# Performance work log

Hardware: AMD Instinct MI355X
Metric: run time of the kernel (lower is better)

## Reference

```python
import jax, jax.numpy as jnp
import numpy as np

CODEBOOK_SIZE = 8192
DIM = 64
B, N = 4, 4096


def setup_inputs() -> dict:
    key = jax.random.key(0)
    k1, k2 = jax.random.split(key)
    x = jax.random.normal(k1, (B, N, DIM), dtype=jnp.float32)
    node_mask = jnp.ones((B, N), dtype=jnp.float32)
    embed = jax.random.normal(k2, (CODEBOOK_SIZE, DIM), dtype=jnp.float32)
    return {"x": x, "node_mask": node_mask, "embed": embed}


def reference(x, node_mask, embed):
    # x: [B, N, D]; embed: [K, D]; node_mask: [B, N]
    b, n, d = x.shape
    k = embed.shape[0]
    flatten = x.reshape(-1, d)  # [B*N, D]
    dist = -(
        jnp.sum(flatten * flatten, axis=1, keepdims=True)
        - 2.0 * (flatten @ embed.T)
        + jnp.sum(embed * embed, axis=1)[None, :]
    )
    embed_ind = jnp.argmax(dist, axis=-1)  # [B*N] nearest-code assignment
    quantize = embed[embed_ind].reshape(b, n, d)  # codebook gather
    # masked one-hot stats (embed_onehot * node_mask), via segment_sum
    mask_flat = node_mask.reshape(-1)
    counts = jax.ops.segment_sum(mask_flat, embed_ind, num_segments=k)  # [K]
    avg_probs = counts / jnp.asarray(flatten.shape[0], dtype=x.dtype)
    perplexity = jnp.exp(-jnp.sum(avg_probs * jnp.log(avg_probs + 1e-10)))
    return quantize, embed_ind.reshape(b, n), perplexity
```

## Files before the change

kernel.cpp:

```cpp
#include <hip/hip_runtime.h>

typedef __attribute__((ext_vector_type(8))) short short8;
typedef __attribute__((ext_vector_type(4))) float f32x4;

#define ROWS 16384
#define DIM 64
#define NCODES 8192
#define MARGIN 0.008f
#define KT_FB 256
#define CTS_PER_BLOCK 32
#define CHUNK 4

#define WS_BEST   0
#define WS_COUNTS 131072
#define WS_ENH    163840
#define WS_ESWZ   196608
#define WS_NEED   2293760

__device__ __forceinline__ unsigned long long pack_score(float s, int idx) {
  unsigned u = __float_as_uint(s);
  u ^= (unsigned)((int)u >> 31) | 0x80000000u;
  return ((unsigned long long)u << 32) | (unsigned)(0xFFFF - idx);
}
__device__ __forceinline__ unsigned short bf16hi(float f) {
  unsigned u = __float_as_uint(f);
  return (unsigned short)((u + 0x7FFFu + ((u >> 16) & 1u)) >> 16);
}

__global__ void vq_enorm(const float* __restrict__ embed, float* __restrict__ enh) {
  int k = blockIdx.x * 256 + threadIdx.x;
  const float4* e4 = (const float4*)(embed + (size_t)k * DIM);
  float a = 0.f, b = 0.f, c = 0.f, d = 0.f;
#pragma unroll
  for (int i = 0; i < DIM / 4; ++i) {
    float4 v = e4[i];
    a = fmaf(v.x, v.x, a); b = fmaf(v.y, v.y, b);
    c = fmaf(v.z, v.z, c); d = fmaf(v.w, v.w, d);
  }
  enh[k] = 0.5f * ((a + b) + (c + d));
}

__global__ void vq_prep_e(const float* __restrict__ embed, short* __restrict__ eswz) {
  int u = blockIdx.x * 256 + threadIdx.x;
  int l = u & 63, kc = (u >> 6) & 1, ct = u >> 7;
  int code = ct * 16 + (l & 15);
  int kb = kc * 32 + (l >> 4) * 8;
  const float* er = embed + (size_t)code * DIM + kb;
  short8 h8, l8;
#pragma unroll
  for (int j = 0; j < 8; ++j) {
    float v = er[j];
    unsigned short h = bf16hi(v);
    float r = v - __uint_as_float((unsigned)h << 16);
    h8[j] = (short)h;
    l8[j] = (short)bf16hi(r);
  }
  short8* dst = (short8*)eswz;
  size_t frag = (size_t)ct * 4 + kc * 2;
  dst[(frag + 0) * 64 + l] = h8;
  dst[(frag + 1) * 64 + l] = l8;
}

__global__ __launch_bounds__(256, 4) void vq_screen(
    const float* __restrict__ x, const float* __restrict__ embed,
    const short* __restrict__ eswz, const float* __restrict__ enh,
    unsigned long long* __restrict__ best) {
  const int t = threadIdx.x;
  const int l = t & 63, wid = t >> 6;
  const int cl = l & 15, grp = l >> 4;
  const int row0 = blockIdx.x * 128 + wid * 32;
  const int ct0 = blockIdx.y * CTS_PER_BLOCK;

  __shared__ short8 bstage[2][CHUNK * 4 * 64];
  __shared__ float enh_s[CTS_PER_BLOCK * 16];

  const char* gbase = (const char*)eswz + (size_t)ct0 * 4 * 1024;

  {
    char* lb = (char*)&bstage[0][0];
#pragma unroll
    for (int i = 0; i < 4; ++i) {
      const int e = i * 256 + t;
      __builtin_amdgcn_global_load_lds(
          (const __attribute__((address_space(1))) void*)(gbase + (size_t)e * 16),
          (__attribute__((address_space(3))) void*)(lb + e * 16), 16, 0, 0);
    }
  }

  enh_s[t] = enh[ct0 * 16 + t];
  enh_s[256 + t] = enh[ct0 * 16 + 256 + t];

  short8 ahi[2][2], alo[2][2];
#pragma unroll
  for (int s = 0; s < 2; ++s) {
    const float4* xr4 = (const float4*)(x + (size_t)(row0 + s * 16 + cl) * DIM);
#pragma unroll
    for (int kc = 0; kc < 2; ++kc) {
      const int q = kc * 8 + grp * 2;
      float4 v0 = xr4[q], v1 = xr4[q + 1];
      float vv[8] = {v0.x, v0.y, v0.z, v0.w, v1.x, v1.y, v1.z, v1.w};
#pragma unroll
      for (int j = 0; j < 8; ++j) {
        unsigned short h = bf16hi(vv[j]);
        float r = vv[j] - __uint_as_float((unsigned)h << 16);
        ahi[s][kc][j] = (short)h;
        alo[s][kc][j] = (short)bf16hi(r);
      }
    }
  }

  float bsc[2][4];
  int bidx[2][4];
#pragma unroll
  for (int s = 0; s < 2; ++s)
#pragma unroll
    for (int j = 0; j < 4; ++j) { bsc[s][j] = -3.4e38f; bidx[s][j] = 0; }

  __syncthreads();

#pragma unroll
  for (int ch = 0; ch < CTS_PER_BLOCK / CHUNK; ++ch) {
    const int cur = ch & 1;
    if (ch + 1 < CTS_PER_BLOCK / CHUNK) {
      const char* gb = gbase + (size_t)(ch + 1) * CHUNK * 4 * 1024;
      char* lb = (char*)&bstage[cur ^ 1][0];
#pragma unroll
      for (int i = 0; i < 4; ++i) {
        const int e = i * 256 + t;
        __builtin_amdgcn_global_load_lds(
            (const __attribute__((address_space(1))) void*)(gb + (size_t)e * 16),
            (__attribute__((address_space(3))) void*)(lb + e * 16), 16, 0, 0);
      }
    }

    const short8* bs = &bstage[cur][0];
#pragma unroll
    for (int ci = 0; ci < CHUNK; ++ci) {
      const int ctl = ch * CHUNK + ci;
      const float eh = enh_s[ctl * 16 + cl];
      short8 h0 = bs[(ci * 4 + 0) * 64 + l], l0 = bs[(ci * 4 + 1) * 64 + l];
      short8 h1 = bs[(ci * 4 + 2) * 64 + l], l1 = bs[(ci * 4 + 3) * 64 + l];

      f32x4 a00 = {-eh, -eh, -eh, -eh};
      f32x4 a10 = a00;
      f32x4 a01 = {0.f, 0.f, 0.f, 0.f};
      f32x4 a11 = a01;
      a00 = __builtin_amdgcn_mfma_f32_16x16x32_bf16(ahi[0][0], h0, a00, 0, 0, 0);
      a10 = __builtin_amdgcn_mfma_f32_16x16x32_bf16(ahi[1][0], h0, a10, 0, 0, 0);
      a01 = __builtin_amdgcn_mfma_f32_16x16x32_bf16(ahi[0][1], h1, a01, 0, 0, 0);
      a11 = __builtin_amdgcn_mfma_f32_16x16x32_bf16(ahi[1][1], h1, a11, 0, 0, 0);
      a00 = __builtin_amdgcn_mfma_f32_16x16x32_bf16(alo[0][0], h0, a00, 0, 0, 0);
      a10 = __builtin_amdgcn_mfma_f32_16x16x32_bf16(alo[1][0], h0, a10, 0, 0, 0);
      a01 = __builtin_amdgcn_mfma_f32_16x16x32_bf16(alo[0][1], h1, a01, 0, 0, 0);
      a11 = __builtin_amdgcn_mfma_f32_16x16x32_bf16(alo[1][1], h1, a11, 0, 0, 0);
      a00 = __builtin_amdgcn_mfma_f32_16x16x32_bf16(ahi[0][0], l0, a00, 0, 0, 0);
      a10 = __builtin_amdgcn_mfma_f32_16x16x32_bf16(ahi[1][0], l0, a10, 0, 0, 0);
      a01 = __builtin_amdgcn_mfma_f32_16x16x32_bf16(ahi[0][1], l1, a01, 0, 0, 0);
      a11 = __builtin_amdgcn_mfma_f32_16x16x32_bf16(ahi[1][1], l1, a11, 0, 0, 0);

      f32x4 s0 = a00 + a01;
      f32x4 s1 = a10 + a11;
      const int code = (ct0 + ctl) * 16 + cl;
#pragma unroll
      for (int j = 0; j < 4; ++j) {
        if (s0[j] > bsc[0][j]) { bsc[0][j] = s0[j]; bidx[0][j] = code; }
        if (s1[j] > bsc[1][j]) { bsc[1][j] = s1[j]; bidx[1][j] = code; }
      }
    }
    __syncthreads();
  }

  unsigned fmask = 0;
#pragma unroll
  for (int s = 0; s < 2; ++s)
#pragma unroll
    for (int j = 0; j < 4; ++j) {
      float m = bsc[s][j];
      m = fmaxf(m, __shfl_xor(m, 1));
      m = fmaxf(m, __shfl_xor(m, 2));
      m = fmaxf(m, __shfl_xor(m, 4));
      m = fmaxf(m, __shfl_xor(m, 8));
      if (bsc[s][j] >= m - MARGIN) fmask |= 1u << (s * 4 + j);
    }

  float exact[2][4];
#pragma unroll
  for (int s = 0; s < 2; ++s)
#pragma unroll
    for (int j = 0; j < 4; ++j) exact[s][j] = -3.4e38f;

  while (__any((int)(fmask != 0))) {
    const bool act = fmask != 0;
    const int sel = act ? __ffs(fmask) - 1 : 0;
    int code = 0;
#pragma unroll
    for (int s = 0; s < 2; ++s)
#pragma unroll
      for (int j = 0; j < 4; ++j)
        code = (sel == s * 4 + j) ? bidx[s][j] : code;
    int row = act ? (row0 + (sel >> 2) * 16 + grp * 4 + (sel & 3)) : row0;
    if (!act) code = 0;
    const float4* xr = (const float4*)(x + (size_t)row * DIM);
    const float4* er = (const float4*)(embed + (size_t)code * DIM);
    float a0 = 0, a1 = 0, a2 = 0, a3 = 0, n0 = 0, n1 = 0, n2 = 0, n3 = 0;
#pragma unroll
    for (int i = 0; i < 16; ++i) {
      float4 xv = xr[i], ev = er[i];
      a0 = fmaf(xv.x, ev.x, a0); a1 = fmaf(xv.y, ev.y, a1);
      a2 = fmaf(xv.z, ev.z, a2); a3 = fmaf(xv.w, ev.w, a3);
      n0 = fmaf(ev.x, ev.x, n0); n1 = fmaf(ev.y, ev.y, n1);
      n2 = fmaf(ev.z, ev.z, n2); n3 = fmaf(ev.w, ev.w, n3);
    }
    float ex = ((a0 + a1) + (a2 + a3)) - 0.5f * ((n0 + n1) + (n2 + n3));
#pragma unroll
    for (int s = 0; s < 2; ++s)
#pragma unroll
      for (int j = 0; j < 4; ++j)
        exact[s][j] = (act && sel == s * 4 + j) ? ex : exact[s][j];
    fmask = act ? (fmask & (fmask - 1)) : 0u;
  }

#pragma unroll
  for (int s = 0; s < 2; ++s)
#pragma unroll
    for (int j = 0; j < 4; ++j) {
      unsigned long long pk = pack_score(exact[s][j], bidx[s][j]);
      unsigned long long o;
      o = __shfl_xor(pk, 1); pk = pk > o ? pk : o;
      o = __shfl_xor(pk, 2); pk = pk > o ? pk : o;
      o = __shfl_xor(pk, 4); pk = pk > o ? pk : o;
      o = __shfl_xor(pk, 8); pk = pk > o ? pk : o;
      if (cl == 0) atomicMax(&best[row0 + s * 16 + grp * 4 + j], pk);
    }
}

__global__ __launch_bounds__(256, 2) void vq_score_fb(
    const float* __restrict__ x, const float* __restrict__ embed,
    const float* __restrict__ enh, unsigned long long* __restrict__ best) {
  const int row = blockIdx.x * 256 + threadIdx.x;
  const int c0 = blockIdx.y * KT_FB;
  float4 xa[16];
  const float4* xg = (const float4*)(x + (size_t)row * DIM);
#pragma unroll
  for (int i = 0; i < 16; ++i) xa[i] = xg[i];
  float bs = -3.4e38f;
  int bc = 0;
#pragma unroll 2
  for (int c = c0; c < c0 + KT_FB; ++c) {
    const float4* e4 = (const float4*)(embed + (size_t)c * DIM);
    float a0 = 0.f, a1 = 0.f, a2 = 0.f, a3 = 0.f;
#pragma unroll
    for (int i = 0; i < 16; ++i) {
      float4 ev = e4[i];
      a0 = fmaf(xa[i].x, ev.x, a0); a1 = fmaf(xa[i].y, ev.y, a1);
      a2 = fmaf(xa[i].z, ev.z, a2); a3 = fmaf(xa[i].w, ev.w, a3);
    }
    float s = ((a0 + a1) + (a2 + a3)) - enh[c];
    if (s > bs) { bs = s; bc = c; }
  }
  atomicMax(&best[row], pack_score(bs, bc));
}

__global__ void vq_finalize(const unsigned long long* __restrict__ best,
                            const float* __restrict__ embed,
                            const float* __restrict__ node_mask,
                            float* __restrict__ quant,
                            float* __restrict__ out_idx,
                            float* __restrict__ counts) {
  int gid = blockIdx.x * 256 + threadIdx.x;
  int row = gid >> 6, d = gid & 63;
  unsigned long long p = best[row];
  int idx = 0xFFFF - (int)(p & 0xFFFFull);
  quant[gid] = embed[(size_t)idx * DIM + d];
  if (d == 0) {
    out_idx[row] = (float)idx;
    atomicAdd(&counts[idx], node_mask[row]);
  }
}

__global__ void vq_perplexity(const float* __restrict__ counts, float* __restrict__ out) {
  int tid = threadIdx.x;
  float acc = 0.f;
  for (int k = tid; k < NCODES; k += 256) {
    float p = counts[k] * (1.0f / (float)ROWS);
    acc += p * logf(p + 1e-10f);
  }
#pragma unroll
  for (int off = 32; off > 0; off >>= 1) acc += __shfl_down(acc, off);
  __shared__ float red[4];
  if ((tid & 63) == 0) red[tid >> 6] = acc;
  __syncthreads();
  if (tid == 0) out[0] = expf(-((red[0] + red[1]) + (red[2] + red[3])));
}

extern "C" void kernel_launch(void* const* d_in, const int* in_sizes, int n_in,
                              void* d_out, int out_size, void* d_ws, size_t ws_size,
                              hipStream_t stream) {
  const float* x = (const float*)d_in[0];
  const float* node_mask = (const float*)d_in[1];
  const float* embed = (const float*)d_in[2];

  float* out = (float*)d_out;
  float* quant = out;
  float* out_idx = out + (size_t)ROWS * DIM;
  float* out_ppl = out_idx + ROWS;

  unsigned long long* best = (unsigned long long*)((char*)d_ws + WS_BEST);
  float* counts = (float*)((char*)d_ws + WS_COUNTS);
  float* enh = (float*)((char*)d_ws + WS_ENH);
  short* eswz = (short*)((char*)d_ws + WS_ESWZ);

  hipMemsetAsync(d_ws, 0, WS_ENH, stream);
  vq_enorm<<<NCODES / 256, 256, 0, stream>>>(embed, enh);
  if (ws_size >= WS_NEED) {
    vq_prep_e<<<256, 256, 0, stream>>>(embed, eswz);
    vq_screen<<<dim3(ROWS / 128, NCODES / (CTS_PER_BLOCK * 16)), 256, 0, stream>>>(
        x, embed, eswz, enh, best);
  } else {
    vq_score_fb<<<dim3(ROWS / 256, NCODES / KT_FB), 256, 0, stream>>>(x, embed, enh, best);
  }
  vq_finalize<<<ROWS * DIM / 256, 256, 0, stream>>>(best, embed, node_mask, quant, out_idx, counts);
  vq_perplexity<<<1, 256, 0, stream>>>(counts, out_ppl);
}
```

Measured before the change: 108.0 us.

## Replace LDS-staged codebook pipeline with direct register prefetch from global

The screening kernel no longer stages swizzled codebook fragments through double-buffered LDS with global_load_lds and block barriers. Each wave now loads its B fragments and norms straight from global memory into registers, prefetching the next code tile one iteration ahead. This removes the LDS traffic and __syncthreads. In exchange, all four waves in a block load the same fragments redundantly from global/L2, and register pressure rises.

```diff
diff --git a/kernel.cpp b/kernel.cpp
--- a/kernel.cpp
+++ b/kernel.cpp
@@ -9,7 +9,6 @@
 #define MARGIN 0.008f
 #define KT_FB 256
 #define CTS_PER_BLOCK 32
-#define CHUNK 4
 
 #define WS_BEST   0
 #define WS_COUNTS 131072
@@ -71,25 +70,6 @@
   const int row0 = blockIdx.x * 128 + wid * 32;
   const int ct0 = blockIdx.y * CTS_PER_BLOCK;
 
-  __shared__ short8 bstage[2][CHUNK * 4 * 64];
-  __shared__ float enh_s[CTS_PER_BLOCK * 16];
-
-  const char* gbase = (const char*)eswz + (size_t)ct0 * 4 * 1024;
-
-  {
-    char* lb = (char*)&bstage[0][0];
-#pragma unroll
-    for (int i = 0; i < 4; ++i) {
-      const int e = i * 256 + t;
-      __builtin_amdgcn_global_load_lds(
-          (const __attribute__((address_space(1))) void*)(gbase + (size_t)e * 16),
-          (__attribute__((address_space(3))) void*)(lb + e * 16), 16, 0, 0);
-    }
-  }
-
-  enh_s[t] = enh[ct0 * 16 + t];
-  enh_s[256 + t] = enh[ct0 * 16 + 256 + t];
-
   short8 ahi[2][2], alo[2][2];
 #pragma unroll
   for (int s = 0; s < 2; ++s) {
@@ -116,58 +96,50 @@
 #pragma unroll
     for (int j = 0; j < 4; ++j) { bsc[s][j] = -3.4e38f; bidx[s][j] = 0; }
 
-  __syncthreads();
-
-#pragma unroll
-  for (int ch = 0; ch < CTS_PER_BLOCK / CHUNK; ++ch) {
-    const int cur = ch & 1;
-    if (ch + 1 < CTS_PER_BLOCK / CHUNK) {
-      const char* gb = gbase + (size_t)(ch + 1) * CHUNK * 4 * 1024;
-      char* lb = (char*)&bstage[cur ^ 1][0];
-#pragma unroll
-      for (int i = 0; i < 4; ++i) {
-        const int e = i * 256 + t;
-        __builtin_amdgcn_global_load_lds(
-            (const __attribute__((address_space(1))) void*)(gb + (size_t)e * 16),
-            (__attribute__((address_space(3))) void*)(lb + e * 16), 16, 0, 0);
-      }
-    }
-
-    const short8* bs = &bstage[cur][0];
-#pragma unroll
-    for (int ci = 0; ci < CHUNK; ++ci) {
-      const int ctl = ch * CHUNK + ci;
-      const float eh = enh_s[ctl * 16 + cl];
-      short8 h0 = bs[(ci * 4 + 0) * 64 + l], l0 = bs[(ci * 4 + 1) * 64 + l];
-      short8 h1 = bs[(ci * 4 + 2) * 64 + l], l1 = bs[(ci * 4 + 3) * 64 + l];
-
-      f32x4 a00 = {-eh, -eh, -eh, -eh};
-      f32x4 a10 = a00;
-      f32x4 a01 = {0.f, 0.f, 0.f, 0.f};
-      f32x4 a11 = a01;
-      a00 = __builtin_amdgcn_mfma_f32_16x16x32_bf16(ahi[0][0], h0, a00, 0, 0, 0);
-      a10 = __builtin_amdgcn_mfma_f32_16x16x32_bf16(ahi[1][0], h0, a10, 0, 0, 0);
-      a01 = __builtin_amdgcn_mfma_f32_16x16x32_bf16(ahi[0][1], h1, a01, 0, 0, 0);
-      a11 = __builtin_amdgcn_mfma_f32_16x16x32_bf16(ahi[1][1], h1, a11, 0, 0, 0);
-      a00 = __builtin_amdgcn_mfma_f32_16x16x32_bf16(alo[0][0], h0, a00, 0, 0, 0);
-      a10 = __builtin_amdgcn_mfma_f32_16x16x32_bf16(alo[1][0], h0, a10, 0, 0, 0);
-      a01 = __builtin_amdgcn_mfma_f32_16x16x32_bf16(alo[0][1], h1, a01, 0, 0, 0);
-      a11 = __builtin_amdgcn_mfma_f32_16x16x32_bf16(alo[1][1], h1, a11, 0, 0, 0);
-      a00 = __builtin_amdgcn_mfma_f32_16x16x32_bf16(ahi[0][0], l0, a00, 0, 0, 0);
-      a10 = __builtin_amdgcn_mfma_f32_16x16x32_bf16(ahi[1][0], l0, a10, 0, 0, 0);
-      a01 = __builtin_amdgcn_mfma_f32_16x16x32_bf16(ahi[0][1], l1, a01, 0, 0, 0);
-      a11 = __builtin_amdgcn_mfma_f32_16x16x32_bf16(ahi[1][1], l1, a11, 0, 0, 0);
-
-      f32x4 s0 = a00 + a01;
-      f32x4 s1 = a10 + a11;
-      const int code = (ct0 + ctl) * 16 + cl;
-#pragma unroll
-      for (int j = 0; j < 4; ++j) {
-        if (s0[j] > bsc[0][j]) { bsc[0][j] = s0[j]; bidx[0][j] = code; }
-        if (s1[j] > bsc[1][j]) { bsc[1][j] = s1[j]; bidx[1][j] = code; }
-      }
-    }
-    __syncthreads();
+  const short8* eb = (const short8*)eswz + (size_t)ct0 * 4 * 64;
+
+  short8 h0 = eb[l], l0 = eb[64 + l], h1 = eb[128 + l], l1 = eb[192 + l];
+  float eh = enh[ct0 * 16 + cl];
+
+#pragma unroll
+  for (int ci = 0; ci < CTS_PER_BLOCK; ++ci) {
+    short8 nh0, nl0, nh1, nl1;
+    float neh;
+    if (ci + 1 < CTS_PER_BLOCK) {
+      const short8* nb = eb + (size_t)(ci + 1) * 256;
+      nh0 = nb[l]; nl0 = nb[64 + l]; nh1 = nb[128 + l]; nl1 = nb[192 + l];
+      neh = enh[(ct0 + ci + 1) * 16 + cl];
+    }
+
+    f32x4 a00 = {-eh, -eh, -eh, -eh};
+    f32x4 a10 = a00;
+    f32x4 a01 = {0.f, 0.f, 0.f, 0.f};
+    f32x4 a11 = a01;
+    a00 = __builtin_amdgcn_mfma_f32_16x16x32_bf16(ahi[0][0], h0, a00, 0, 0, 0);
+    a10 = __builtin_amdgcn_mfma_f32_16x16x32_bf16(ahi[1][0], h0, a10, 0, 0, 0);
+    a01 = __builtin_amdgcn_mfma_f32_16x16x32_bf16(ahi[0][1], h1, a01, 0, 0, 0);
+    a11 = __builtin_amdgcn_mfma_f32_16x16x32_bf16(ahi[1][1], h1, a11, 0, 0, 0);
+    a00 = __builtin_amdgcn_mfma_f32_16x16x32_bf16(alo[0][0], h0, a00, 0, 0, 0);
+    a10 = __builtin_amdgcn_mfma_f32_16x16x32_bf16(alo[1][0], h0, a10, 0, 0, 0);
+    a01 = __builtin_amdgcn_mfma_f32_16x16x32_bf16(alo[0][1], h1, a01, 0, 0, 0);
+    a11 = __builtin_amdgcn_mfma_f32_16x16x32_bf16(alo[1][1], h1, a11, 0, 0, 0);
+    a00 = __builtin_amdgcn_mfma_f32_16x16x32_bf16(ahi[0][0], l0, a00, 0, 0, 0);
+    a10 = __builtin_amdgcn_mfma_f32_16x16x32_bf16(ahi[1][0], l0, a10, 0, 0, 0);
+    a01 = __builtin_amdgcn_mfma_f32_16x16x32_bf16(ahi[0][1], l1, a01, 0, 0, 0);
+    a11 = __builtin_amdgcn_mfma_f32_16x16x32_bf16(ahi[1][1], l1, a11, 0, 0, 0);
+
+    f32x4 s0 = a00 + a01;
+    f32x4 s1 = a10 + a11;
+    const int code = (ct0 + ci) * 16 + cl;
+#pragma unroll
+    for (int j = 0; j < 4; ++j) {
+      if (s0[j] > bsc[0][j]) { bsc[0][j] = s0[j]; bidx[0][j] = code; }
+      if (s1[j] > bsc[1][j]) { bsc[1][j] = s1[j]; bidx[1][j] = code; }
+    }
+
+    if (ci + 1 < CTS_PER_BLOCK) {
+      h0 = nh0; l0 = nl0; h1 = nh1; l1 = nl1; eh = neh;
+    }
   }
 
   unsigned fmask = 0;
```

Measured after the change: 118.5 us. 1.1x slower.

## Halve rows per wave in screen kernel to raise occupancy

Applied to the files above, without the earlier changes.

Each wave in vq_screen now handles 16 rows instead of 32, so it keeps half the A fragments and best-score registers. The launch bound rises to 8 blocks per CU and the grid doubles. The LDS stage shrinks to 2 code tiles per chunk, the chunk loop is no longer unrolled, and code norms are read straight from global memory instead of a shared copy. In exchange, each B fragment loaded from LDS is reused by half as many MFMAs, and the codebook is streamed twice as many times overall.

```diff
diff --git a/kernel.cpp b/kernel.cpp
--- a/kernel.cpp
+++ b/kernel.cpp
@@ -9,7 +9,7 @@
 #define MARGIN 0.008f
 #define KT_FB 256
 #define CTS_PER_BLOCK 32
-#define CHUNK 4
+#define CCH 2
 
 #define WS_BEST   0
 #define WS_COUNTS 131072
@@ -61,25 +61,24 @@
   dst[(frag + 1) * 64 + l] = l8;
 }
 
-__global__ __launch_bounds__(256, 4) void vq_screen(
+__global__ __launch_bounds__(256, 8) void vq_screen(
     const float* __restrict__ x, const float* __restrict__ embed,
     const short* __restrict__ eswz, const float* __restrict__ enh,
     unsigned long long* __restrict__ best) {
   const int t = threadIdx.x;
   const int l = t & 63, wid = t >> 6;
   const int cl = l & 15, grp = l >> 4;
-  const int row0 = blockIdx.x * 128 + wid * 32;
+  const int row0 = blockIdx.x * 64 + wid * 16;
   const int ct0 = blockIdx.y * CTS_PER_BLOCK;
 
-  __shared__ short8 bstage[2][CHUNK * 4 * 64];
-  __shared__ float enh_s[CTS_PER_BLOCK * 16];
+  __shared__ short8 bstage[2][CCH * 4 * 64];
 
   const char* gbase = (const char*)eswz + (size_t)ct0 * 4 * 1024;
 
   {
     char* lb = (char*)&bstage[0][0];
 #pragma unroll
-    for (int i = 0; i < 4; ++i) {
+    for (int i = 0; i < CCH; ++i) {
       const int e = i * 256 + t;
       __builtin_amdgcn_global_load_lds(
           (const __attribute__((address_space(1))) void*)(gbase + (size_t)e * 16),
@@ -87,13 +86,9 @@
     }
   }
 
-  enh_s[t] = enh[ct0 * 16 + t];
-  enh_s[256 + t] = enh[ct0 * 16 + 256 + t];
-
-  short8 ahi[2][2], alo[2][2];
-#pragma unroll
-  for (int s = 0; s < 2; ++s) {
-    const float4* xr4 = (const float4*)(x + (size_t)(row0 + s * 16 + cl) * DIM);
+  short8 ahi[2], alo[2];
+  {
+    const float4* xr4 = (const float4*)(x + (size_t)(row0 + cl) * DIM);
 #pragma unroll
     for (int kc = 0; kc < 2; ++kc) {
       const int q = kc * 8 + grp * 2;
@@ -103,29 +98,26 @@
       for (int j = 0; j < 8; ++j) {
         unsigned short h = bf16hi(vv[j]);
         float r = vv[j] - __uint_as_float((unsigned)h << 16);
-        ahi[s][kc][j] = (short)h;
-        alo[s][kc][j] = (short)bf16hi(r);
+        ahi[kc][j] = (short)h;
+        alo[kc][j] = (short)bf16hi(r);
       }
     }
   }
 
-  float bsc[2][4];
-  int bidx[2][4];
-#pragma unroll
-  for (int s = 0; s < 2; ++s)
-#pragma unroll
-    for (int j = 0; j < 4; ++j) { bsc[s][j] = -3.4e38f; bidx[s][j] = 0; }
+  float bsc[4];
+  int bidx[4];
+#pragma unroll
+  for (int j = 0; j < 4; ++j) { bsc[j] = -3.4e38f; bidx[j] = 0; }
 
   __syncthreads();
 
-#pragma unroll
-  for (int ch = 0; ch < CTS_PER_BLOCK / CHUNK; ++ch) {
+  for (int ch = 0; ch < CTS_PER_BLOCK / CCH; ++ch) {
     const int cur = ch & 1;
-    if (ch + 1 < CTS_PER_BLOCK / CHUNK) {
-      const char* gb = gbase + (size_t)(ch + 1) * CHUNK * 4 * 1024;
+    if (ch + 1 < CTS_PER_BLOCK / CCH) {
+      const char* gb = gbase + (size_t)(ch + 1) * CCH * 4 * 1024;
       char* lb = (char*)&bstage[cur ^ 1][0];
 #pragma unroll
-      for (int i = 0; i < 4; ++i) {
+      for (int i = 0; i < CCH; ++i) {
         const int e = i * 256 + t;
         __builtin_amdgcn_global_load_lds(
             (const __attribute__((address_space(1))) void*)(gb + (size_t)e * 16),
@@ -135,36 +127,24 @@
 
     const short8* bs = &bstage[cur][0];
 #pragma unroll
-    for (int ci = 0; ci < CHUNK; ++ci) {
-      const int ctl = ch * CHUNK + ci;
-      const float eh = enh_s[ctl * 16 + cl];
-      short8 h0 = bs[(ci * 4 + 0) * 64 + l], l0 = bs[(ci * 4 + 1) * 64 + l];
-      short8 h1 = bs[(ci * 4 + 2) * 64 + l], l1 = bs[(ci * 4 + 3) * 64 + l];
-
-      f32x4 a00 = {-eh, -eh, -eh, -eh};
-      f32x4 a10 = a00;
-      f32x4 a01 = {0.f, 0.f, 0.f, 0.f};
-      f32x4 a11 = a01;
-      a00 = __builtin_amdgcn_mfma_f32_16x16x32_bf16(ahi[0][0], h0, a00, 0, 0, 0);
-      a10 = __builtin_amdgcn_mfma_f32_16x16x32_bf16(ahi[1][0], h0, a10, 0, 0, 0);
-      a01 = __builtin_amdgcn_mfma_f32_16x16x32_bf16(ahi[0][1], h1, a01, 0, 0, 0);
-      a11 = __builtin_amdgcn_mfma_f32_16x16x32_bf16(ahi[1][1], h1, a11, 0, 0, 0);
-      a00 = __builtin_amdgcn_mfma_f32_16x16x32_bf16(alo[0][0], h0, a00, 0, 0, 0);
-      a10 = __builtin_amdgcn_mfma_f32_16x16x32_bf16(alo[1][0], h0, a10, 0, 0, 0);
-      a01 = __builtin_amdgcn_mfma_f32_16x16x32_bf16(alo[0][1], h1, a01, 0, 0, 0);
-      a11 = __builtin_amdgcn_mfma_f32_16x16x32_bf16(alo[1][1], h1, a11, 0, 0, 0);
-      a00 = __builtin_amdgcn_mfma_f32_16x16x32_bf16(ahi[0][0], l0, a00, 0, 0, 0);
-      a10 = __builtin_amdgcn_mfma_f32_16x16x32_bf16(ahi[1][0], l0, a10, 0, 0, 0);
-      a01 = __builtin_amdgcn_mfma_f32_16x16x32_bf16(ahi[0][1], l1, a01, 0, 0, 0);
-      a11 = __builtin_amdgcn_mfma_f32_16x16x32_bf16(ahi[1][1], l1, a11, 0, 0, 0);
-
-      f32x4 s0 = a00 + a01;
-      f32x4 s1 = a10 + a11;
-      const int code = (ct0 + ctl) * 16 + cl;
+    for (int cil = 0; cil < CCH; ++cil) {
+      const int ci = ch * CCH + cil;
+      const float eh = enh[(ct0 + ci) * 16 + cl];
+      short8 h0 = bs[(cil * 4 + 0) * 64 + l], l0 = bs[(cil * 4 + 1) * 64 + l];
+      short8 h1 = bs[(cil * 4 + 2) * 64 + l], l1 = bs[(cil * 4 + 3) * 64 + l];
+
+      f32x4 acc = {-eh, -eh, -eh, -eh};
+      acc = __builtin_amdgcn_mfma_f32_16x16x32_bf16(ahi[0], h0, acc, 0, 0, 0);
+      acc = __builtin_amdgcn_mfma_f32_16x16x32_bf16(alo[0], h0, acc, 0, 0, 0);
+      acc = __builtin_amdgcn_mfma_f32_16x16x32_bf16(ahi[0], l0, acc, 0, 0, 0);
+      acc = __builtin_amdgcn_mfma_f32_16x16x32_bf16(ahi[1], h1, acc, 0, 0, 0);
+      acc = __builtin_amdgcn_mfma_f32_16x16x32_bf16(alo[1], h1, acc, 0, 0, 0);
+      acc = __builtin_amdgcn_mfma_f32_16x16x32_bf16(ahi[1], l1, acc, 0, 0, 0);
+
+      const int code = (ct0 + ci) * 16 + cl;
 #pragma unroll
       for (int j = 0; j < 4; ++j) {
-        if (s0[j] > bsc[0][j]) { bsc[0][j] = s0[j]; bidx[0][j] = code; }
-        if (s1[j] > bsc[1][j]) { bsc[1][j] = s1[j]; bidx[1][j] = code; }
+        if (acc[j] > bsc[j]) { bsc[j] = acc[j]; bidx[j] = code; }
       }
     }
     __syncthreads();
@@ -172,33 +152,26 @@
 
   unsigned fmask = 0;
 #pragma unroll
-  for (int s = 0; s < 2; ++s)
-#pragma unroll
-    for (int j = 0; j < 4; ++j) {
-      float m = bsc[s][j];
-      m = fmaxf(m, __shfl_xor(m, 1));
-      m = fmaxf(m, __shfl_xor(m, 2));
-      m = fmaxf(m, __shfl_xor(m, 4));
-      m = fmaxf(m, __shfl_xor(m, 8));
-      if (bsc[s][j] >= m - MARGIN) fmask |= 1u << (s * 4 + j);
-    }
-
-  float exact[2][4];
-#pragma unroll
-  for (int s = 0; s < 2; ++s)
-#pragma unroll
-    for (int j = 0; j < 4; ++j) exact[s][j] = -3.4e38f;
+  for (int j = 0; j < 4; ++j) {
+    float m = bsc[j];
+    m = fmaxf(m, __shfl_xor(m, 1));
+    m = fmaxf(m, __shfl_xor(m, 2));
+    m = fmaxf(m, __shfl_xor(m, 4));
+    m = fmaxf(m, __shfl_xor(m, 8));
+    if (bsc[j] >= m - MARGIN) fmask |= 1u << j;
+  }
+
+  float exact[4];
+#pragma unroll
+  for (int j = 0; j < 4; ++j) exact[j] = -3.4e38f;
 
   while (__any((int)(fmask != 0))) {
     const bool act = fmask != 0;
     const int sel = act ? __ffs(fmask) - 1 : 0;
     int code = 0;
 #pragma unroll
-    for (int s = 0; s < 2; ++s)
-#pragma unroll
-      for (int j = 0; j < 4; ++j)
-        code = (sel == s * 4 + j) ? bidx[s][j] : code;
-    int row = act ? (row0 + (sel >> 2) * 16 + grp * 4 + (sel & 3)) : row0;
+    for (int j = 0; j < 4; ++j) code = (sel == j) ? bidx[j] : code;
+    int row = act ? (row0 + grp * 4 + sel) : row0;
     if (!act) code = 0;
     const float4* xr = (const float4*)(x + (size_t)row * DIM);
     const float4* er = (const float4*)(embed + (size_t)code * DIM);
@@ -213,25 +186,21 @@
     }
     float ex = ((a0 + a1) + (a2 + a3)) - 0.5f * ((n0 + n1) + (n2 + n3));
 #pragma unroll
-    for (int s = 0; s < 2; ++s)
-#pragma unroll
-      for (int j = 0; j < 4; ++j)
-        exact[s][j] = (act && sel == s * 4 + j) ? ex : exact[s][j];
+    for (int j = 0; j < 4; ++j)
+      exact[j] = (act && sel == j) ? ex : exact[j];
     fmask = act ? (fmask & (fmask - 1)) : 0u;
   }
 
 #pragma unroll
-  for (int s = 0; s < 2; ++s)
-#pragma unroll
-    for (int j = 0; j < 4; ++j) {
-      unsigned long long pk = pack_score(exact[s][j], bidx[s][j]);
-      unsigned long long o;
-      o = __shfl_xor(pk, 1); pk = pk > o ? pk : o;
-      o = __shfl_xor(pk, 2); pk = pk > o ? pk : o;
-      o = __shfl_xor(pk, 4); pk = pk > o ? pk : o;
-      o = __shfl_xor(pk, 8); pk = pk > o ? pk : o;
-      if (cl == 0) atomicMax(&best[row0 + s * 16 + grp * 4 + j], pk);
-    }
+  for (int j = 0; j < 4; ++j) {
+    unsigned long long pk = pack_score(exact[j], bidx[j]);
+    unsigned long long o;
+    o = __shfl_xor(pk, 1); pk = pk > o ? pk : o;
+    o = __shfl_xor(pk, 2); pk = pk > o ? pk : o;
+    o = __shfl_xor(pk, 4); pk = pk > o ? pk : o;
+    o = __shfl_xor(pk, 8); pk = pk > o ? pk : o;
+    if (cl == 0) atomicMax(&best[row0 + grp * 4 + j], pk);
+  }
 }
 
 __global__ __launch_bounds__(256, 2) void vq_score_fb(
@@ -314,7 +283,7 @@
   vq_enorm<<<NCODES / 256, 256, 0, stream>>>(embed, enh);
   if (ws_size >= WS_NEED) {
     vq_prep_e<<<256, 256, 0, stream>>>(embed, eswz);
-    vq_screen<<<dim3(ROWS / 128, NCODES / (CTS_PER_BLOCK * 16)), 256, 0, stream>>>(
+    vq_screen<<<dim3(ROWS / 64, NCODES / (CTS_PER_BLOCK * 16)), 256, 0, stream>>>(
         x, embed, eswz, enh, best);
   } else {
     vq_score_fb<<<dim3(ROWS / 256, NCODES / KT_FB), 256, 0, stream>>>(x, embed, enh, best);
```

After: 118.9 us. +10.1%, slower.
